# Kernel optimization log

Hardware: AMD Instinct MI355X
Metric: run time of the kernel (lower is better)

## Reference

```python
import jax, jax.numpy as jnp
import numpy as np

N, L, E, H, D = 4, 2048, 1024, 16, 64

def setup_inputs() -> dict:
    key = jax.random.key(0)
    ks = jax.random.split(key, 8)
    s = 1.0 / np.sqrt(E)
    return {
        "Q": jax.random.normal(ks[0], (N, L, E), jnp.float32),
        "K": jax.random.normal(ks[1], (N, L, E), jnp.float32),
        "V": jax.random.normal(ks[2], (N, L, E), jnp.float32),
        "Wq": jax.random.normal(ks[3], (H * D, E), jnp.float32) * s,
        "bq": jnp.zeros((H * D,), jnp.float32),
        "Wk": jax.random.normal(ks[4], (H * D, E), jnp.float32) * s,
        "bk": jnp.zeros((H * D,), jnp.float32),
        "Wv": jax.random.normal(ks[5], (H * D, E), jnp.float32) * s,
        "bv": jnp.zeros((H * D,), jnp.float32),
        "Wo": jax.random.normal(ks[6], (E, H * D), jnp.float32) * s,
        "bo": jnp.zeros((E,), jnp.float32),
    }

def reference(Q, K, V, Wq, bq, Wk, bk, Wv, bv, Wo, bo):
    n, lq, e = Q.shape
    lk = K.shape[1]
    # projections: Linear(x) = x @ W.T + b
    q = (Q @ Wq.T + bq).reshape(n, lq, H, D)
    k = (K @ Wk.T + bk).reshape(n, lk, H, D)
    v = (V @ Wv.T + bv).reshape(n, lk, H, D)
    # scores over key dim (original broadcasts Q*K and sums over d)
    scores = jnp.einsum('nqhd,nkhd->nqkh', q, k) / jnp.sqrt(jnp.float32(D))
    attn = jax.nn.softmax(scores, axis=2)  # softmax over key axis
    out = jnp.einsum('nqkh,nkhd->nqhd', attn, v)
    out = out.reshape(n, lq, H * D)
    return (out @ Wo.T + bo).reshape(n, lq, E)
```

## Files before the change

kernel.cpp:

```cpp
#include <hip/hip_runtime.h>
#include <cstdint>
#include <cstddef>


typedef __bf16 bf16x8 __attribute__((ext_vector_type(8)));
typedef __bf16 bf16x4 __attribute__((ext_vector_type(4)));
typedef __bf16 bf16x2 __attribute__((ext_vector_type(2)));
typedef float f32x4 __attribute__((ext_vector_type(4)));
typedef float f32x2 __attribute__((ext_vector_type(2)));
typedef unsigned int uint2v __attribute__((ext_vector_type(2)));
typedef unsigned int uint4v __attribute__((ext_vector_type(4)));

#define LOG2E_OVER_SQRTD 0.18033688011112042f

__device__ __forceinline__ unsigned short f2bf(float f) {
  unsigned int u = __builtin_bit_cast(unsigned int, f);
  u = (u + 0x7fffu + ((u >> 16) & 1u)) >> 16;
  return (unsigned short)u;
}

__device__ __forceinline__ unsigned int pk2(float a, float b) {
  f32x2 t = {a, b};
  bf16x2 h = __builtin_convertvector(t, bf16x2);
  return __builtin_bit_cast(unsigned int, h);
}

__device__ __forceinline__ void gl2lds16(const void* g, void* l) {
  __builtin_amdgcn_global_load_lds(
      (__attribute__((address_space(1))) unsigned int*)g,
      (__attribute__((address_space(3))) unsigned int*)l, 16, 0, 0);
}

__device__ __forceinline__ bf16x8 mk_ap(f32x4 sA, f32x4 sB) {
  float peA[4], peB[4];
#pragma unroll
  for (int r = 0; r < 4; ++r) {
    peA[r] = __builtin_amdgcn_exp2f(sA[r]);
    peB[r] = __builtin_amdgcn_exp2f(sB[r]);
  }
  unsigned int x00 = pk2(peA[0], peA[1]);
  unsigned int x01 = pk2(peA[2], peA[3]);
  unsigned int x10 = pk2(peB[0], peB[1]);
  unsigned int x11 = pk2(peB[2], peB[3]);
  uint2v s0 = __builtin_amdgcn_permlane32_swap(x00, x10, false, false);
  uint2v t0 = __builtin_amdgcn_permlane16_swap(s0[0], s0[1], false, false);
  uint2v s1 = __builtin_amdgcn_permlane32_swap(x01, x11, false, false);
  uint2v t1 = __builtin_amdgcn_permlane16_swap(s1[0], s1[1], false, false);
  uint4v u;
  u[0] = t0[0];
  u[1] = t1[0];
  u[2] = t0[1];
  u[3] = t1[1];
  return __builtin_bit_cast(bf16x8, u);
}

struct CvtArgs {
  const float* src[7];
  unsigned short* dst[7];
};
__global__ __launch_bounds__(256) void cvt_all_k(CvtArgs a) {
  int bid = blockIdx.x;
  int which, x;
  if (bid < 24576) {
    which = bid >> 13;
    x = bid & 8191;
  } else {
    int r = bid - 24576;
    which = 3 + (r >> 10);
    x = r & 1023;
  }
  const float* s = a.src[which];
  unsigned short* d = a.dst[which];
  size_t i = ((size_t)x * 256 + threadIdx.x) * 4;
  float4 v = *(const float4*)(s + i);
  ushort4 o;
  o.x = f2bf(v.x); o.y = f2bf(v.y); o.z = f2bf(v.z); o.w = f2bf(v.w);
  *(ushort4*)(d + i) = o;
}

struct GemmDesc {
  const unsigned short* A;
  const unsigned short* Bt;
  const float* bias;
  void* C;
  int N;
  int nbx_shift;
  float scale;
  int bias_row;
  int permc;
};
struct GemmPack3 {
  GemmDesc g[3];
};

template <bool OUT_F32>
__global__ __launch_bounds__(256, 3) void gemm_multi_k(GemmPack3 p) {
  __shared__ __attribute__((aligned(16))) unsigned short As[128 * 64];
  __shared__ __attribute__((aligned(16))) unsigned short Bs[128 * 64];
  const GemmDesc d = p.g[blockIdx.x >> 9];
  int t = blockIdx.x & 511;
  if (d.nbx_shift == 3) t = ((t & 7) << 6) | (t >> 3);
  const int bx = t & ((1 << d.nbx_shift) - 1);
  const int by = t >> d.nbx_shift;

  const int tid = threadIdx.x;
  const int lane = tid & 63, wave = tid >> 6;
  const int lr = lane & 15, lg = lane >> 4;
  const int rowBase = by * 128;
  const int colBase = bx * 128;
  const int wm = (wave & 1) * 64, wn = (wave >> 1) * 64;

  f32x4 acc[4][4] = {};

  const unsigned short* gA[4];
  const unsigned short* gB[4];
  unsigned short* lA[4];
  unsigned short* lB[4];
#pragma unroll
  for (int i = 0; i < 4; ++i) {
    int s = tid + i * 256;
    int row = s >> 3;
    int c = (s & 7) ^ (row & 7);
    gA[i] = d.A + (size_t)(rowBase + row) * 1024 + c * 8;
    gB[i] = d.Bt + (size_t)(colBase + row) * 1024 + c * 8;
    lA[i] = &As[s * 8];
    lB[i] = &Bs[s * 8];
  }

  for (int kt = 0; kt < 16; ++kt) {
    const int ko = kt * 64;
#pragma unroll
    for (int i = 0; i < 4; ++i) {
      gl2lds16(gA[i] + ko, lA[i]);
      gl2lds16(gB[i] + ko, lB[i]);
    }
    __syncthreads();

#pragma unroll
    for (int ks = 0; ks < 2; ++ks) {
      bf16x8 af[4], bfr[4];
#pragma unroll
      for (int mt = 0; mt < 4; ++mt) {
        int row = wm + mt * 16 + lr;
        int c = (ks * 4 + lg) ^ (row & 7);
        af[mt] = *(const bf16x8*)&As[row * 64 + c * 8];
      }
#pragma unroll
      for (int nt = 0; nt < 4; ++nt) {
        int row = wn + nt * 16 + lr;
        int c = (ks * 4 + lg) ^ (row & 7);
        bfr[nt] = *(const bf16x8*)&Bs[row * 64 + c * 8];
      }
#pragma unroll
      for (int mt = 0; mt < 4; ++mt)
#pragma unroll
        for (int nt = 0; nt < 4; ++nt)
          acc[mt][nt] = __builtin_amdgcn_mfma_f32_16x16x32_bf16(
              af[mt], bfr[nt], acc[mt][nt], 0, 0, 0);
    }
    __syncthreads();
  }

#pragma unroll
  for (int mt = 0; mt < 4; ++mt)
#pragma unroll
    for (int nt = 0; nt < 4; ++nt) {
      int col = colBase + wn + nt * 16 + lr;
      int colStore = d.permc ? (colBase + wn + lr * 4 + nt) : col;
      float bcol = d.bias_row ? 0.f : d.bias[col];
#pragma unroll
      for (int r = 0; r < 4; ++r) {
        int row = rowBase + wm + mt * 16 + lg * 4 + r;
        float b = d.bias_row ? d.bias[row] : bcol;
        float val = (acc[mt][nt][r] + b) * d.scale;
        size_t idx = (size_t)row * (size_t)d.N + (size_t)colStore;
        if (OUT_F32)
          ((float*)d.C)[idx] = val;
        else
          ((unsigned short*)d.C)[idx] = f2bf(val);
      }
    }
}

__global__ __launch_bounds__(256, 4) void attn_k(
    const unsigned short* __restrict__ qb,
    const unsigned short* __restrict__ kb,
    const unsigned short* __restrict__ vtb,
    unsigned short* __restrict__ aob) {
  __shared__ __attribute__((aligned(16))) unsigned short Ks[2 * 64 * 64];
  __shared__ __attribute__((aligned(16))) unsigned short Vts[2 * 64 * 64];

  const int tid = threadIdx.x;
  const int lane = tid & 63, wave = tid >> 6;
  const int lr = lane & 15, lg = lane >> 4;

  const int bid = blockIdx.x;
  const int xcd = bid & 7;
  const int idx = bid >> 3;
  const int qt = idx & 15;
  const int nh = (idx >> 4) * 8 + xcd;
  const int h = nh & 15, n = nh >> 4;
  const int q0 = qt * 128;

#pragma unroll
  for (int i = 0; i < 4; ++i) {
    int s = i * 256 + tid;
    int row = s >> 3;
    int c = (s & 7) ^ (row & 7);
    gl2lds16(qb + (((size_t)n * 2048 + q0 + row) << 10) + h * 64 + c * 8,
             &Ks[s * 8]);
  }
  __syncthreads();

  bf16x8 aq[2][2];
#pragma unroll
  for (int mt = 0; mt < 2; ++mt)
#pragma unroll
    for (int ks = 0; ks < 2; ++ks) {
      int row = wave * 32 + mt * 16 + lr;
      int c = (ks * 4 + lg) ^ (row & 7);
      aq[mt][ks] = *(const bf16x8*)&Ks[row * 64 + c * 8];
    }
  __syncthreads();

  const int a0 = lr * 64 + ((lg ^ (lr & 7)) * 8);
  const int a1 = lr * 64 + (((4 + lg) ^ (lr & 7)) * 8);
  const unsigned short* Kb0 = &Ks[a0];
  const unsigned short* Kb1 = &Ks[a1];
  const unsigned short* Vb0 = &Vts[a0];
  const unsigned short* Vb1 = &Vts[a1];

  const unsigned short* kg[2];
  const unsigned short* vg[2];
  int ldo[2];
#pragma unroll
  for (int i = 0; i < 2; ++i) {
    int s = i * 256 + tid;
    int row = s >> 3;
    int c = (s & 7) ^ (row & 7);
    kg[i] = kb + (((size_t)n * 2048 + row) << 10) + h * 64 + c * 8;
    vg[i] = vtb + (((size_t)(h * 64 + row)) << 13) + (size_t)n * 2048 + c * 8;
    ldo[i] = s * 8;
  }
#pragma unroll
  for (int i = 0; i < 2; ++i) {
    gl2lds16(kg[i], &Ks[ldo[i]]);
    gl2lds16(vg[i], &Vts[ldo[i]]);
    kg[i] += 64 * 1024;
    vg[i] += 64;
  }

  bf16x8 ones;
#pragma unroll
  for (int i = 0; i < 8; ++i) ones[i] = (__bf16)1.0f;
  const f32x4 fzero = {0.f, 0.f, 0.f, 0.f};

  f32x4 o_acc[2][4] = {};
  f32x4 o_sum[2] = {};

#pragma unroll 2
  for (int kt = 0; kt < 32; ++kt) {
    const int cb = (kt & 1) * 4096;
    const int nb = 4096 - cb;
    __syncthreads();

    if (kt < 31) {
#pragma unroll
      for (int i = 0; i < 2; ++i) {
        gl2lds16(kg[i], &Ks[nb + ldo[i]]);
        gl2lds16(vg[i], &Vts[nb + ldo[i]]);
        kg[i] += 64 * 1024;
        vg[i] += 64;
      }
    }

    f32x4 sA[2][2], sB[2][2];
    {
      bf16x8 k00 = *(const bf16x8*)(Kb0 + cb);
      bf16x8 k10 = *(const bf16x8*)(Kb1 + cb);
      bf16x8 k01 = *(const bf16x8*)(Kb0 + cb + 1024);
      bf16x8 k11 = *(const bf16x8*)(Kb1 + cb + 1024);
      __builtin_amdgcn_s_setprio(1);
#pragma unroll
      for (int mt = 0; mt < 2; ++mt) {
        f32x4 t0 = __builtin_amdgcn_mfma_f32_16x16x32_bf16(
            k00, aq[mt][0], fzero, 0, 0, 0);
        sA[mt][0] = __builtin_amdgcn_mfma_f32_16x16x32_bf16(
            k10, aq[mt][1], t0, 0, 0, 0);
        f32x4 t1 = __builtin_amdgcn_mfma_f32_16x16x32_bf16(
            k01, aq[mt][0], fzero, 0, 0, 0);
        sA[mt][1] = __builtin_amdgcn_mfma_f32_16x16x32_bf16(
            k11, aq[mt][1], t1, 0, 0, 0);
      }
      __builtin_amdgcn_s_setprio(0);
    }
    {
      bf16x8 k02 = *(const bf16x8*)(Kb0 + cb + 2048);
      bf16x8 k12 = *(const bf16x8*)(Kb1 + cb + 2048);
      bf16x8 k03 = *(const bf16x8*)(Kb0 + cb + 3072);
      bf16x8 k13 = *(const bf16x8*)(Kb1 + cb + 3072);
      __builtin_amdgcn_s_setprio(1);
#pragma unroll
      for (int mt = 0; mt < 2; ++mt) {
        f32x4 t0 = __builtin_amdgcn_mfma_f32_16x16x32_bf16(
            k02, aq[mt][0], fzero, 0, 0, 0);
        sB[mt][0] = __builtin_amdgcn_mfma_f32_16x16x32_bf16(
            k12, aq[mt][1], t0, 0, 0, 0);
        f32x4 t1 = __builtin_amdgcn_mfma_f32_16x16x32_bf16(
            k03, aq[mt][0], fzero, 0, 0, 0);
        sB[mt][1] = __builtin_amdgcn_mfma_f32_16x16x32_bf16(
            k13, aq[mt][1], t1, 0, 0, 0);
      }
      __builtin_amdgcn_s_setprio(0);
    }

    {
      bf16x8 bv0[4];
#pragma unroll
      for (int nt = 0; nt < 4; ++nt)
        bv0[nt] = *(const bf16x8*)(Vb0 + cb + nt * 1024);

      bf16x8 ap0[2];
#pragma unroll
      for (int mt = 0; mt < 2; ++mt) ap0[mt] = mk_ap(sA[mt][0], sA[mt][1]);

      __builtin_amdgcn_s_setprio(1);
#pragma unroll
      for (int mt = 0; mt < 2; ++mt) {
        o_sum[mt] = __builtin_amdgcn_mfma_f32_16x16x32_bf16(
            ap0[mt], ones, o_sum[mt], 0, 0, 0);
#pragma unroll
        for (int nt = 0; nt < 4; ++nt)
          o_acc[mt][nt] = __builtin_amdgcn_mfma_f32_16x16x32_bf16(
              ap0[mt], bv0[nt], o_acc[mt][nt], 0, 0, 0);
      }
      __builtin_amdgcn_s_setprio(0);
    }

    {
      bf16x8 bv1[4];
#pragma unroll
      for (int nt = 0; nt < 4; ++nt)
        bv1[nt] = *(const bf16x8*)(Vb1 + cb + nt * 1024);

      bf16x8 ap1[2];
#pragma unroll
      for (int mt = 0; mt < 2; ++mt) ap1[mt] = mk_ap(sB[mt][0], sB[mt][1]);

      __builtin_amdgcn_s_setprio(1);
#pragma unroll
      for (int mt = 0; mt < 2; ++mt) {
        o_sum[mt] = __builtin_amdgcn_mfma_f32_16x16x32_bf16(
            ap1[mt], ones, o_sum[mt], 0, 0, 0);
#pragma unroll
        for (int nt = 0; nt < 4; ++nt)
          o_acc[mt][nt] = __builtin_amdgcn_mfma_f32_16x16x32_bf16(
              ap1[mt], bv1[nt], o_acc[mt][nt], 0, 0, 0);
      }
      __builtin_amdgcn_s_setprio(0);
    }
  }

#pragma unroll
  for (int mt = 0; mt < 2; ++mt) {
#pragma unroll
    for (int r = 0; r < 4; ++r) {
      float inv = 1.0f / o_sum[mt][r];
      int row_l = q0 + wave * 32 + mt * 16 + lg * 4 + r;
      size_t base = (((size_t)n * 2048 + row_l) << 10) + h * 64;
#pragma unroll
      for (int nt = 0; nt < 4; ++nt)
        aob[base + nt * 16 + lr] = f2bf(o_acc[mt][nt][r] * inv);
    }
  }
}

extern "C" void kernel_launch(void* const* d_in, const int* in_sizes, int n_in,
                              void* d_out, int out_size, void* d_ws,
                              size_t ws_size, hipStream_t stream) {
  const float* Q = (const float*)d_in[0];
  const float* K = (const float*)d_in[1];
  const float* V = (const float*)d_in[2];
  const float* Wq = (const float*)d_in[3];
  const float* bq = (const float*)d_in[4];
  const float* Wk = (const float*)d_in[5];
  const float* bk = (const float*)d_in[6];
  const float* Wv = (const float*)d_in[7];
  const float* bv = (const float*)d_in[8];
  const float* Wo = (const float*)d_in[9];
  const float* bo = (const float*)d_in[10];

  const size_t S = (size_t)8192 * 1024;
  const size_t W = (size_t)1024 * 1024;
  unsigned short* ws = (unsigned short*)d_ws;
  unsigned short* Qbf = ws;
  unsigned short* Kbf = ws + S;
  unsigned short* Vbf = ws + 2 * S;
  unsigned short* qbuf = ws + 3 * S;
  unsigned short* kbuf = ws + 4 * S;
  unsigned short* vtbuf = ws + 5 * S;
  unsigned short* Wqb = ws + 6 * S;
  unsigned short* Wkb = Wqb + W;
  unsigned short* Wvb = Wqb + 2 * W;
  unsigned short* Wob = Wqb + 3 * W;
  unsigned short* aob = Qbf;

  CvtArgs cv;
  cv.src[0] = Q;  cv.dst[0] = Qbf;
  cv.src[1] = K;  cv.dst[1] = Kbf;
  cv.src[2] = V;  cv.dst[2] = Vbf;
  cv.src[3] = Wq; cv.dst[3] = Wqb;
  cv.src[4] = Wk; cv.dst[4] = Wkb;
  cv.src[5] = Wv; cv.dst[5] = Wvb;
  cv.src[6] = Wo; cv.dst[6] = Wob;
  cvt_all_k<<<28672, 256, 0, stream>>>(cv);

  GemmPack3 pp;
  pp.g[0] = {Qbf, Wqb, bq, qbuf, 1024, 3, LOG2E_OVER_SQRTD, 0, 0};
  pp.g[1] = {Kbf, Wkb, bk, kbuf, 1024, 3, 1.0f, 0, 0};
  pp.g[2] = {Wvb, Vbf, bv, vtbuf, 8192, 6, 1.0f, 1, 0};
  gemm_multi_k<false><<<1536, 256, 0, stream>>>(pp);

  attn_k<<<1024, 256, 0, stream>>>(qbuf, kbuf, vtbuf, aob);

  GemmPack3 po;
  po.g[0] = {aob, Wob, bo, d_out, 1024, 3, 1.0f, 0, 0};
  po.g[1] = po.g[0];
  po.g[2] = po.g[0];
  gemm_multi_k<true><<<512, 256, 0, stream>>>(po);
}
```

Before: 332.8 us.

## Fuse fp32-to-bf16 conversion of activations into the projection GEMM loads

```diff
diff --git a/kernel.cpp b/kernel.cpp
--- a/kernel.cpp
+++ b/kernel.cpp
@@ -55,23 +55,13 @@
 }
 
 struct CvtArgs {
-  const float* src[7];
-  unsigned short* dst[7];
+  const float* src[4];
+  unsigned short* dst[4];
 };
-__global__ __launch_bounds__(256) void cvt_all_k(CvtArgs a) {
-  int bid = blockIdx.x;
-  int which, x;
-  if (bid < 24576) {
-    which = bid >> 13;
-    x = bid & 8191;
-  } else {
-    int r = bid - 24576;
-    which = 3 + (r >> 10);
-    x = r & 1023;
-  }
-  const float* s = a.src[which];
-  unsigned short* d = a.dst[which];
-  size_t i = ((size_t)x * 256 + threadIdx.x) * 4;
+__global__ __launch_bounds__(256) void cvt_w_k(CvtArgs a) {
+  const float* s = a.src[blockIdx.y];
+  unsigned short* d = a.dst[blockIdx.y];
+  size_t i = ((size_t)blockIdx.x * 256 + threadIdx.x) * 4;
   float4 v = *(const float4*)(s + i);
   ushort4 o;
   o.x = f2bf(v.x); o.y = f2bf(v.y); o.z = f2bf(v.z); o.w = f2bf(v.w);
@@ -88,13 +78,15 @@
   float scale;
   int bias_row;
   int permc;
+  int a_f32;
+  int b_f32;
 };
 struct GemmPack3 {
   GemmDesc g[3];
 };
 
 template <bool OUT_F32>
-__global__ __launch_bounds__(256, 3) void gemm_multi_k(GemmPack3 p) {
+__global__ __launch_bounds__(256, 4) void gemm_multi_k(GemmPack3 p) {
   __shared__ __attribute__((aligned(16))) unsigned short As[128 * 64];
   __shared__ __attribute__((aligned(16))) unsigned short Bs[128 * 64];
   const GemmDesc d = p.g[blockIdx.x >> 9];
@@ -113,7 +105,9 @@
   f32x4 acc[4][4] = {};
 
   const unsigned short* gA[4];
+  const float* gAf[4];
   const unsigned short* gB[4];
+  const float* gBf[4];
   unsigned short* lA[4];
   unsigned short* lB[4];
 #pragma unroll
@@ -121,18 +115,49 @@
     int s = tid + i * 256;
     int row = s >> 3;
     int c = (s & 7) ^ (row & 7);
-    gA[i] = d.A + (size_t)(rowBase + row) * 1024 + c * 8;
-    gB[i] = d.Bt + (size_t)(colBase + row) * 1024 + c * 8;
+    size_t offA = (size_t)(rowBase + row) * 1024 + c * 8;
+    size_t offB = (size_t)(colBase + row) * 1024 + c * 8;
+    gA[i] = d.A + offA;
+    gAf[i] = (const float*)(const void*)d.A + offA;
+    gB[i] = d.Bt + offB;
+    gBf[i] = (const float*)(const void*)d.Bt + offB;
     lA[i] = &As[s * 8];
     lB[i] = &Bs[s * 8];
   }
 
   for (int kt = 0; kt < 16; ++kt) {
     const int ko = kt * 64;
-#pragma unroll
-    for (int i = 0; i < 4; ++i) {
-      gl2lds16(gA[i] + ko, lA[i]);
-      gl2lds16(gB[i] + ko, lB[i]);
+    if (d.a_f32) {
+#pragma unroll
+      for (int i = 0; i < 4; ++i) {
+        float4 a0 = *(const float4*)(gAf[i] + ko);
+        float4 a1 = *(const float4*)(gAf[i] + ko + 4);
+        uint4v u;
+        u[0] = pk2(a0.x, a0.y);
+        u[1] = pk2(a0.z, a0.w);
+        u[2] = pk2(a1.x, a1.y);
+        u[3] = pk2(a1.z, a1.w);
+        *(uint4v*)lA[i] = u;
+      }
+    } else {
+#pragma unroll
+      for (int i = 0; i < 4; ++i) gl2lds16(gA[i] + ko, lA[i]);
+    }
+    if (d.b_f32) {
+#pragma unroll
+      for (int i = 0; i < 4; ++i) {
+        float4 b0 = *(const float4*)(gBf[i] + ko);
+        float4 b1 = *(const float4*)(gBf[i] + ko + 4);
+        uint4v u;
+        u[0] = pk2(b0.x, b0.y);
+        u[1] = pk2(b0.z, b0.w);
+        u[2] = pk2(b1.x, b1.y);
+        u[3] = pk2(b1.z, b1.w);
+        *(uint4v*)lB[i] = u;
+      }
+    } else {
+#pragma unroll
+      for (int i = 0; i < 4; ++i) gl2lds16(gB[i] + ko, lB[i]);
     }
     __syncthreads();
 
@@ -393,9 +418,7 @@
   const size_t S = (size_t)8192 * 1024;
   const size_t W = (size_t)1024 * 1024;
   unsigned short* ws = (unsigned short*)d_ws;
-  unsigned short* Qbf = ws;
-  unsigned short* Kbf = ws + S;
-  unsigned short* Vbf = ws + 2 * S;
+  unsigned short* aob = ws;
   unsigned short* qbuf = ws + 3 * S;
   unsigned short* kbuf = ws + 4 * S;
   unsigned short* vtbuf = ws + 5 * S;
@@ -403,28 +426,27 @@
   unsigned short* Wkb = Wqb + W;
   unsigned short* Wvb = Wqb + 2 * W;
   unsigned short* Wob = Wqb + 3 * W;
-  unsigned short* aob = Qbf;
-
-  CvtArgs cv;
-  cv.src[0] = Q;  cv.dst[0] = Qbf;
-  cv.src[1] = K;  cv.dst[1] = Kbf;
-  cv.src[2] = V;  cv.dst[2] = Vbf;
-  cv.src[3] = Wq; cv.dst[3] = Wqb;
-  cv.src[4] = Wk; cv.dst[4] = Wkb;
-  cv.src[5] = Wv; cv.dst[5] = Wvb;
-  cv.src[6] = Wo; cv.dst[6] = Wob;
-  cvt_all_k<<<28672, 256, 0, stream>>>(cv);
+
+  CvtArgs cw;
+  cw.src[0] = Wq; cw.dst[0] = Wqb;
+  cw.src[1] = Wk; cw.dst[1] = Wkb;
+  cw.src[2] = Wv; cw.dst[2] = Wvb;
+  cw.src[3] = Wo; cw.dst[3] = Wob;
+  cvt_w_k<<<dim3(1024, 4), 256, 0, stream>>>(cw);
 
   GemmPack3 pp;
-  pp.g[0] = {Qbf, Wqb, bq, qbuf, 1024, 3, LOG2E_OVER_SQRTD, 0, 0};
-  pp.g[1] = {Kbf, Wkb, bk, kbuf, 1024, 3, 1.0f, 0, 0};
-  pp.g[2] = {Wvb, Vbf, bv, vtbuf, 8192, 6, 1.0f, 1, 0};
+  pp.g[0] = {(const unsigned short*)(const void*)Q, Wqb, bq, qbuf,
+             1024, 3, LOG2E_OVER_SQRTD, 0, 0, 1, 0};
+  pp.g[1] = {(const unsigned short*)(const void*)K, Wkb, bk, kbuf,
+             1024, 3, 1.0f, 0, 0, 1, 0};
+  pp.g[2] = {Wvb, (const unsigned short*)(const void*)V, bv, vtbuf,
+             8192, 6, 1.0f, 1, 0, 0, 1};
   gemm_multi_k<false><<<1536, 256, 0, stream>>>(pp);
 
   attn_k<<<1024, 256, 0, stream>>>(qbuf, kbuf, vtbuf, aob);
 
   GemmPack3 po;
-  po.g[0] = {aob, Wob, bo, d_out, 1024, 3, 1.0f, 0, 0};
+  po.g[0] = {aob, Wob, bo, d_out, 1024, 3, 1.0f, 0, 0, 0, 0};
   po.g[1] = po.g[0];
   po.g[2] = po.g[0];
   gemm_multi_k<true><<<512, 256, 0, stream>>>(po);
```

Measured after the change: 394.6 us. 18.6% more time.
